# Performance work log

Hardware: AMD Instinct MI355X
Metric: run time of the kernel (lower is better)

## Reference

```python
import jax, jax.numpy as jnp
import numpy as np

NEG_SLOPE = 0.2


def gat_layer(x, adj, W, a_src, a_dst):
    # x: (C, in_dim), adj: (C, C) 0/1, W: (in_dim, H*D), a_src/a_dst: (H, D)
    C = x.shape[0]
    H, D = a_src.shape
    h = (x @ W).reshape(C, H, D)            # (C, H, D)
    hh = jnp.transpose(h, (1, 0, 2))        # (H, C, D)
    asrc = jnp.einsum('hcd,hd->hc', hh, a_src)  # (H, C)
    adst = jnp.einsum('hcd,hd->hc', hh, a_dst)  # (H, C)
    e = asrc[:, :, None] + adst[:, None, :]     # (H, C, C)
    e = jax.nn.leaky_relu(e, NEG_SLOPE)
    e = jnp.where(adj[None, :, :] == 0, -jnp.inf, e)
    attn = jax.nn.softmax(e, axis=-1)           # (H, C, C)
    out = jnp.einsum('hij,hjd->hid', attn, hh)  # (H, C, D)
    return jnp.transpose(out, (1, 0, 2)).reshape(C, H * D)


def setup_inputs() -> dict:
    key = jax.random.key(0)
    ks = jax.random.split(key, 12)
    B, doc_dim = 1024, 768
    C, label_dim = 4096, 768
    hidden, H = 512, 4
    D = hidden // H  # 128

    doc_x = jax.random.normal(ks[0], (B, doc_dim), dtype=jnp.float32)
    label_init = jax.random.normal(ks[1], (C, label_dim), dtype=jnp.float32)
    adj = jax.random.randint(ks[2], (C, C), 0, 2, dtype=jnp.int32)
    adj = adj.at[jnp.arange(C), jnp.arange(C)].set(1)  # self-loops

    def xavier(k, shape):
        fan_in, fan_out = shape[0], shape[1]
        lim = jnp.sqrt(6.0 / (fan_in + fan_out)).astype(jnp.float32)
        return jax.random.uniform(k, shape, jnp.float32, -lim, lim)

    W1 = xavier(ks[3], (label_dim, hidden))
    a_src1 = xavier(ks[4], (H, D))
    a_dst1 = xavier(ks[5], (H, D))
    W2 = xavier(ks[6], (hidden, hidden))
    a_src2 = xavier(ks[7], (H, D))
    a_dst2 = xavier(ks[8], (H, D))
    Wd = xavier(ks[9], (doc_dim, hidden))
    bd = jnp.zeros((hidden,), jnp.float32)
    return {"doc_x": doc_x, "label_init": label_init, "adj": adj,
            "W1": W1, "a_src1": a_src1, "a_dst1": a_dst1,
            "W2": W2, "a_src2": a_src2, "a_dst2": a_dst2,
            "Wd": Wd, "bd": bd}


def reference(doc_x, label_init, adj, W1, a_src1, a_dst1, W2, a_src2, a_dst2, Wd, bd):
    # doc_proj (dropout = identity in eval)
    doc_h = jax.nn.relu(doc_x @ Wd + bd)            # (B, hidden)
    # label encoder: GAT -> ELU -> GAT
    h = gat_layer(label_init, adj, W1, a_src1, a_dst1)
    h = jax.nn.elu(h)
    label_h = gat_layer(h, adj, W2, a_src2, a_dst2)  # (C, hidden)
    logits = doc_h @ label_h.T                      # (B, C)
    return logits
```

## Files before the change

kernel.cpp:

```cpp
#include <hip/hip_runtime.h>
#include <hip/hip_bf16.h>
#include <math.h>

#define BDOCS   1024
#define CNODES  4096
#define INDIM   768
#define HID     512
#define NHEAD   4
#define HDIM    128
#define NEG_SLOPE 0.2f

typedef __attribute__((ext_vector_type(8))) short short8;
typedef __attribute__((ext_vector_type(4))) float f32x4;

__device__ __forceinline__ float lrelu(float x) { return x > 0.f ? x : NEG_SLOPE * x; }

__device__ __forceinline__ short f2bf(float f) {
    union { float f; unsigned u; } v; v.f = f;
    unsigned r = (v.u + 0x7fff + ((v.u >> 16) & 1)) >> 16;
    return (short)r;
}
__device__ __forceinline__ float bf2f(short s) {
    union { float f; unsigned u; } v; v.u = ((unsigned)(unsigned short)s) << 16;
    return v.f;
}

__global__ __launch_bounds__(256)
void pack_adj(const int* __restrict__ adj, unsigned long long* __restrict__ adjb64)
{
    const int t    = threadIdx.x;
    const int gw   = blockIdx.x * 4 + (t >> 6);
    const int lane = t & 63;
    const int i  = gw >> 6;
    const int j0 = (gw & 63) * 64;
    const int a  = adj[(size_t)i * CNODES + j0 + lane];
    const unsigned long long m = __ballot(a != 0);
    if (lane == 0) adjb64[(size_t)i * 64 + (j0 >> 6)] = m;
}

__global__ __launch_bounds__(512)
void attn_prep(const float* __restrict__ hpre,
               const float* __restrict__ a_src,
               const float* __restrict__ a_dst,
               float* __restrict__ asrc, float* __restrict__ adst)
{
    const int i = blockIdx.x;
    const int t = threadIdx.x;
    __shared__ float s1[512], s2[512];
    const float hv = hpre[(size_t)i * HID + t];
    s1[t] = hv * a_src[t];
    s2[t] = hv * a_dst[t];
    __syncthreads();
    for (int s = 64; s >= 1; s >>= 1) {
        if ((t & 127) < s) { s1[t] += s1[t + s]; s2[t] += s2[t + s]; }
        __syncthreads();
    }
    if ((t & 127) == 0) {
        const int h = t >> 7;
        asrc[h * CNODES + i] = s1[t];
        adst[h * CNODES + i] = s2[t];
    }
}

__global__ __launch_bounds__(256)
void adst_max(const float* __restrict__ adst, float* __restrict__ Mh)
{
    const int h = blockIdx.x, t = threadIdx.x;
    __shared__ float red[256];
    float m = -1e30f;
    for (int j = t; j < CNODES; j += 256) m = fmaxf(m, adst[h * CNODES + j]);
    red[t] = m; __syncthreads();
    for (int s = 128; s >= 1; s >>= 1) {
        if (t < s) red[t] = fmaxf(red[t], red[t + s]);
        __syncthreads();
    }
    if (t == 0) Mh[h] = red[0];
}

__global__ __launch_bounds__(256)
void frag_T(const float* __restrict__ src, short* __restrict__ dst, int N, int K)
{
    __shared__ float tile[32][132];
    const int jc = blockIdx.x;
    const int nq = blockIdx.y;
    const int t  = threadIdx.x;
    const int KC = K >> 5;
#pragma unroll
    for (int it = 0; it < 16; it++) {
        const int e = it * 256 + t;
        const int j = e >> 7, n = e & 127;
        tile[j][n] = src[(size_t)(jc * 32 + j) * N + nq * 128 + n];
    }
    __syncthreads();
#pragma unroll
    for (int s = 0; s < 2; s++) {
        const int item = s * 256 + t;
        const int nbl = item >> 6, lane = item & 63;
        const int nr = lane & 15, kq = lane >> 4;
        short8 v;
#pragma unroll
        for (int jr = 0; jr < 8; jr++)
            v[jr] = f2bf(tile[kq * 8 + jr][nbl * 16 + nr]);
        *(short8*)&dst[((size_t)((nq * 8 + nbl) * KC + jc) * 64 + lane) * 8] = v;
    }
}

template <bool ELU>
__global__ __launch_bounds__(256)
void frag_A(const float* __restrict__ src, short* __restrict__ dst, int C)
{
    __shared__ float tile[16][132];
    const int rb = blockIdx.x, cq = blockIdx.y;
    const int t  = threadIdx.x;
    const int KC = C >> 5;
#pragma unroll
    for (int it = 0; it < 8; it++) {
        const int e = it * 256 + t;
        const int r = e >> 7, c = e & 127;
        float v = src[(size_t)(rb * 16 + r) * C + cq * 128 + c];
        if (ELU) v = v > 0.f ? v : (__expf(v) - 1.f);
        tile[r][c] = v;
    }
    __syncthreads();
    const int kcl = t >> 6, lane = t & 63;
    const int m = lane & 15, kq = lane >> 4;
    short8 v8;
#pragma unroll
    for (int j = 0; j < 8; j++) v8[j] = f2bf(tile[m][kcl * 32 + kq * 8 + j]);
    *(short8*)&dst[((size_t)(rb * KC + cq * 4 + kcl) * 64 + lane) * 8] = v8;
}

template <int KC, bool BIASRELU>
__global__ __launch_bounds__(64, 3)
void gemm_frag(const short* __restrict__ Af, const short* __restrict__ Bf,
               const float* __restrict__ bias, float* __restrict__ Cmat, int N)
{
    const int lane = threadIdx.x;
    const int mb0  = blockIdx.x * 2;
    const int nq   = blockIdx.y;

    f32x4 acc[2][8];
#pragma unroll
    for (int f = 0; f < 2; f++)
#pragma unroll
        for (int c = 0; c < 8; c++) acc[f][c] = (f32x4){0.f, 0.f, 0.f, 0.f};

    const short* ap0 = Af + (size_t)mb0 * KC * 512 + lane * 8;
    const short* ap1 = ap0 + (size_t)KC * 512;
    const short* bp  = Bf + (size_t)(nq * 8) * KC * 512 + lane * 8;

#pragma unroll 2
    for (int kc = 0; kc < KC; kc++) {
        short8 a0 = *(const short8*)(ap0 + (size_t)kc * 512);
        short8 a1 = *(const short8*)(ap1 + (size_t)kc * 512);
        short8 bf[8];
#pragma unroll
        for (int c = 0; c < 8; c++)
            bf[c] = *(const short8*)(bp + ((size_t)c * KC + kc) * 512);
#pragma unroll
        for (int c = 0; c < 8; c++) {
            acc[0][c] = __builtin_amdgcn_mfma_f32_16x16x32_bf16(a0, bf[c], acc[0][c], 0, 0, 0);
            acc[1][c] = __builtin_amdgcn_mfma_f32_16x16x32_bf16(a1, bf[c], acc[1][c], 0, 0, 0);
        }
    }

    const int col = lane & 15, q4 = lane >> 4;
#pragma unroll
    for (int f = 0; f < 2; f++)
#pragma unroll
        for (int c = 0; c < 8; c++)
#pragma unroll
            for (int r = 0; r < 4; r++) {
                const int row = (mb0 + f) * 16 + q4 * 4 + r;
                const int n   = nq * 128 + c * 16 + col;
                float v = acc[f][c][r];
                if (BIASRELU) v = fmaxf(v + bias[n], 0.f);
                Cmat[(size_t)row * N + n] = v;
            }
}

__global__ __launch_bounds__(256, 3)
void attn_pv(const short* __restrict__ hbTf,
             const unsigned int* __restrict__ adjb,
             const float* __restrict__ asrc, const float* __restrict__ adst,
             const float* __restrict__ Mh,
             float* __restrict__ part, float* __restrict__ lpart,
             int jper)
{
    const int t    = threadIdx.x;
    const int w    = t >> 6;
    const int lane = t & 63;
    const int m    = lane & 15;
    const int kq   = lane >> 4;
    const int i0   = blockIdx.x * 32;
    const int ks   = blockIdx.y;
    const int js   = ks * jper;

    const float as0 = asrc[w * CNODES + i0 + m];
    const float as1 = asrc[w * CNODES + i0 + 16 + m];
    const float mh  = Mh[w];
    const float mr0 = lrelu(as0 + mh);
    const float mr1 = lrelu(as1 + mh);
    float ls0 = 0.f, ls1 = 0.f;

    f32x4 acc[2][8];
#pragma unroll
    for (int f = 0; f < 2; f++)
#pragma unroll
        for (int c = 0; c < 8; c++) acc[f][c] = (f32x4){0.f, 0.f, 0.f, 0.f};

    const unsigned int* ar0 = adjb + (size_t)(i0 + m) * 128 + (js >> 5);
    const unsigned int* ar1 = adjb + (size_t)(i0 + 16 + m) * 128 + (js >> 5);
    const int nchunks = jper >> 5;

    for (int ch = 0; ch < nchunks; ch++) {
        const int j0 = js + ch * 32;
        const unsigned int aw0 = ar0[ch] >> (kq * 8);
        const unsigned int aw1 = ar1[ch] >> (kq * 8);
        const float4* dp = (const float4*)(adst + (size_t)w * CNODES + j0 + kq * 8);
        const float4 d0 = dp[0], d1 = dp[1];

        short8 bf[8];
        const short* bbase = hbTf + (((size_t)(w * 8) * 128 + (j0 >> 5)) * 64 + lane) * 8;
#pragma unroll
        for (int c = 0; c < 8; c++)
            bf[c] = *(const short8*)(bbase + (size_t)c * 128 * 64 * 8);

        const float dv[8] = {d0.x, d0.y, d0.z, d0.w, d1.x, d1.y, d1.z, d1.w};
        short8 a0, a1;
#pragma unroll
        for (int q = 0; q < 8; q++) {
            const unsigned b0 = (aw0 >> q) & 1u, b1 = (aw1 >> q) & 1u;
            float w0 = b0 ? __expf(lrelu(as0 + dv[q]) - mr0) : 0.f;
            float w1 = b1 ? __expf(lrelu(as1 + dv[q]) - mr1) : 0.f;
            short r0 = f2bf(w0), r1 = f2bf(w1);
            a0[q] = r0; a1[q] = r1;
            ls0 += bf2f(r0); ls1 += bf2f(r1);
        }

#pragma unroll
        for (int c = 0; c < 8; c++) {
            acc[0][c] = __builtin_amdgcn_mfma_f32_16x16x32_bf16(a0, bf[c], acc[0][c], 0, 0, 0);
            acc[1][c] = __builtin_amdgcn_mfma_f32_16x16x32_bf16(a1, bf[c], acc[1][c], 0, 0, 0);
        }
    }

    ls0 += __shfl_xor(ls0, 16); ls0 += __shfl_xor(ls0, 32);
    ls1 += __shfl_xor(ls1, 16); ls1 += __shfl_xor(ls1, 32);
    if (lane < 16) {
        lpart[((size_t)ks * NHEAD + w) * CNODES + i0 + m]      = ls0;
        lpart[((size_t)ks * NHEAD + w) * CNODES + i0 + 16 + m] = ls1;
    }

    float* pbase = part + (size_t)ks * CNODES * HID;
    const int col = lane & 15, q4 = lane >> 4;
#pragma unroll
    for (int f = 0; f < 2; f++)
#pragma unroll
        for (int c = 0; c < 8; c++)
#pragma unroll
            for (int r = 0; r < 4; r++) {
                const int row = i0 + f * 16 + q4 * 4 + r;
                pbase[(size_t)row * HID + w * HDIM + c * 16 + col] = acc[f][c][r];
            }
}

__global__ __launch_bounds__(256)
void reduce_norm(const float* __restrict__ part, const float* __restrict__ lpart,
                 float* __restrict__ outbuf, int KS)
{
    const int idx = blockIdx.x * 256 + threadIdx.x;
    const int i = idx >> 9, n = idx & 511;
    const int h = n >> 7;
    float l = 0.f, v = 0.f;
    for (int s = 0; s < KS; s++) {
        l += lpart[((size_t)s * NHEAD + h) * CNODES + i];
        v += part[(size_t)s * CNODES * HID + idx];
    }
    outbuf[idx] = v / l;
}

extern "C" void kernel_launch(void* const* d_in, const int* in_sizes, int n_in,
                              void* d_out, int out_size, void* d_ws, size_t ws_size,
                              hipStream_t stream)
{
    const float* doc_x      = (const float*)d_in[0];
    const float* label_init = (const float*)d_in[1];
    const int*   adj        = (const int*)d_in[2];
    const float* W1         = (const float*)d_in[3];
    const float* a_src1     = (const float*)d_in[4];
    const float* a_dst1     = (const float*)d_in[5];
    const float* W2         = (const float*)d_in[6];
    const float* a_src2     = (const float*)d_in[7];
    const float* a_dst2     = (const float*)d_in[8];
    const float* Wd         = (const float*)d_in[9];
    const float* bd         = (const float*)d_in[10];
    float*       out        = (float*)d_out;

    char* wsb = (char*)d_ws;
    size_t off = 0;
    auto alloc = [&](size_t bytes) -> char* {
        char* p = wsb + off;
        off = (off + bytes + 255) & ~(size_t)255;
        return p;
    };

    float* doc_h = (float*)alloc((size_t)BDOCS * HID * 4);
    float* buf1  = (float*)alloc((size_t)CNODES * HID * 4);
    float* buf2  = (float*)alloc((size_t)CNODES * HID * 4);
    float* asrc  = (float*)alloc(NHEAD * CNODES * 4);
    float* adst  = (float*)alloc(NHEAD * CNODES * 4);
    float* Mh    = (float*)alloc(256);
    float* lpart = (float*)alloc((size_t)4 * NHEAD * CNODES * 4);
    unsigned int* adjb = (unsigned int*)alloc((size_t)CNODES * 128 * 4);
    short* hbTf  = (short*)alloc((size_t)CNODES * HID * 2);
    short* Wdf   = (short*)alloc((size_t)INDIM * HID * 2);
    short* W1f   = (short*)alloc((size_t)INDIM * HID * 2);
    short* W2f   = (short*)alloc((size_t)HID * HID * 2);
    short* dxf   = (short*)alloc((size_t)BDOCS * INDIM * 2);
    char*  reg   = alloc((size_t)9 << 20);
    short* Af_li = (short*)reg;
    short* Af2   = (short*)reg;
    short* lhf   = (short*)(reg + ((size_t)4 << 20));
    short* dhf   = (short*)(reg + ((size_t)8 << 20));
    float* part  = (float*)(wsb + off);

    int KS = 4;
    const size_t slice_bytes = (size_t)CNODES * HID * 4;
    while (KS > 1 && off + (size_t)KS * slice_bytes > ws_size) KS >>= 1;
    const int jper = CNODES / KS;

    const dim3 blk(256);

    pack_adj<<<CNODES * CNODES / 64 / 4, blk, 0, stream>>>(adj, (unsigned long long*)adjb);
    frag_T<<<dim3(INDIM / 32, HID / 128), blk, 0, stream>>>(Wd, Wdf, HID, INDIM);
    frag_T<<<dim3(INDIM / 32, HID / 128), blk, 0, stream>>>(W1, W1f, HID, INDIM);
    frag_T<<<dim3(HID / 32, HID / 128), blk, 0, stream>>>(W2, W2f, HID, HID);
    frag_A<false><<<dim3(BDOCS / 16, INDIM / 128), blk, 0, stream>>>(doc_x, dxf, INDIM);
    frag_A<false><<<dim3(CNODES / 16, INDIM / 128), blk, 0, stream>>>(label_init, Af_li, INDIM);

    gemm_frag<INDIM / 32, false><<<dim3(CNODES / 32, HID / 128), 64, 0, stream>>>(Af_li, W1f, nullptr, buf1, HID);

    gemm_frag<INDIM / 32, true><<<dim3(BDOCS / 32, HID / 128), 64, 0, stream>>>(dxf, Wdf, bd, doc_h, HID);
    frag_A<false><<<dim3(BDOCS / 16, HID / 128), blk, 0, stream>>>(doc_h, dhf, HID);

    attn_prep<<<CNODES, 512, 0, stream>>>(buf1, a_src1, a_dst1, asrc, adst);
    adst_max<<<NHEAD, 256, 0, stream>>>(adst, Mh);
    frag_T<<<dim3(CNODES / 32, HID / 128), blk, 0, stream>>>(buf1, hbTf, HID, CNODES);
    attn_pv<<<dim3(CNODES / 32, KS), blk, 0, stream>>>(hbTf, adjb, asrc, adst, Mh, part, lpart, jper);
    reduce_norm<<<CNODES * HID / 256, blk, 0, stream>>>(part, lpart, buf2, KS);

    frag_A<true><<<dim3(CNODES / 16, HID / 128), blk, 0, stream>>>(buf2, Af2, HID);
    gemm_frag<HID / 32, false><<<dim3(CNODES / 32, HID / 128), 64, 0, stream>>>(Af2, W2f, nullptr, buf1, HID);

    attn_prep<<<CNODES, 512, 0, stream>>>(buf1, a_src2, a_dst2, asrc, adst);
    adst_max<<<NHEAD, 256, 0, stream>>>(adst, Mh);
    frag_T<<<dim3(CNODES / 32, HID / 128), blk, 0, stream>>>(buf1, hbTf, HID, CNODES);
    attn_pv<<<dim3(CNODES / 32, KS), blk, 0, stream>>>(hbTf, adjb, asrc, adst, Mh, part, lpart, jper);
    reduce_norm<<<CNODES * HID / 256, blk, 0, stream>>>(part, lpart, buf2, KS);

    frag_A<false><<<dim3(CNODES / 16, HID / 128), blk, 0, stream>>>(buf2, lhf, HID);
    gemm_frag<HID / 32, false><<<dim3(BDOCS / 32, CNODES / 128), 64, 0, stream>>>(dhf, lhf, nullptr, out, CNODES);
}
```

Measured before the change: 371.0 us.

## Fuse GEMM epilogues with attention prep, factor exp out of attention loop

```diff
diff --git a/kernel.cpp b/kernel.cpp
--- a/kernel.cpp
+++ b/kernel.cpp
@@ -20,9 +20,15 @@
     unsigned r = (v.u + 0x7fff + ((v.u >> 16) & 1)) >> 16;
     return (short)r;
 }
-__device__ __forceinline__ float bf2f(short s) {
-    union { float f; unsigned u; } v; v.u = ((unsigned)(unsigned short)s) << 16;
-    return v.f;
+__device__ __forceinline__ unsigned pk2(float a, float b) {
+    union { float f; unsigned u; } x, y; x.f = a; y.f = b;
+    unsigned lo = (x.u + 0x7fff + ((x.u >> 16) & 1)) >> 16;
+    unsigned hi = (y.u + 0x7fff + ((y.u >> 16) & 1)) >> 16;
+    return lo | (hi << 16);
+}
+__device__ __forceinline__ short hup(float f) {
+    union { float f; unsigned u; } v; v.f = f;
+    return (short)((v.u + 0x8000) >> 16);
 }
 
 __global__ __launch_bounds__(256)
@@ -38,28 +44,236 @@
     if (lane == 0) adjb64[(size_t)i * 64 + (j0 >> 6)] = m;
 }
 
-__global__ __launch_bounds__(512)
-void attn_prep(const float* __restrict__ hpre,
-               const float* __restrict__ a_src,
-               const float* __restrict__ a_dst,
-               float* __restrict__ asrc, float* __restrict__ adst)
-{
-    const int i = blockIdx.x;
-    const int t = threadIdx.x;
-    __shared__ float s1[512], s2[512];
-    const float hv = hpre[(size_t)i * HID + t];
-    s1[t] = hv * a_src[t];
-    s2[t] = hv * a_dst[t];
+__global__ __launch_bounds__(256)
+void frag_T(const float* __restrict__ src, short* __restrict__ dst, int N, int K)
+{
+    __shared__ float tile[32][132];
+    const int jc = blockIdx.x;
+    const int nq = blockIdx.y;
+    const int t  = threadIdx.x;
+    const int KC = K >> 5;
+#pragma unroll
+    for (int it = 0; it < 16; it++) {
+        const int e = it * 256 + t;
+        const int j = e >> 7, n = e & 127;
+        tile[j][n] = src[(size_t)(jc * 32 + j) * N + nq * 128 + n];
+    }
     __syncthreads();
-    for (int s = 64; s >= 1; s >>= 1) {
-        if ((t & 127) < s) { s1[t] += s1[t + s]; s2[t] += s2[t + s]; }
-        __syncthreads();
-    }
-    if ((t & 127) == 0) {
-        const int h = t >> 7;
-        asrc[h * CNODES + i] = s1[t];
-        adst[h * CNODES + i] = s2[t];
-    }
+#pragma unroll
+    for (int s = 0; s < 2; s++) {
+        const int item = s * 256 + t;
+        const int nbl = item >> 6, lane = item & 63;
+        const int nr = lane & 15, kq = lane >> 4;
+        short8 v;
+#pragma unroll
+        for (int jr = 0; jr < 8; jr++)
+            v[jr] = f2bf(tile[kq * 8 + jr][nbl * 16 + nr]);
+        *(short8*)&dst[((size_t)((nq * 8 + nbl) * KC + jc) * 64 + lane) * 8] = v;
+    }
+}
+
+__global__ __launch_bounds__(256)
+void frag_A(const float* __restrict__ src, short* __restrict__ dst, int C)
+{
+    __shared__ float tile[16][132];
+    const int rb = blockIdx.x, cq = blockIdx.y;
+    const int t  = threadIdx.x;
+    const int KC = C >> 5;
+#pragma unroll
+    for (int it = 0; it < 8; it++) {
+        const int e = it * 256 + t;
+        const int r = e >> 7, c = e & 127;
+        tile[r][c] = src[(size_t)(rb * 16 + r) * C + cq * 128 + c];
+    }
+    __syncthreads();
+    const int kcl = t >> 6, lane = t & 63;
+    const int m = lane & 15, kq = lane >> 4;
+    short8 v8;
+#pragma unroll
+    for (int j = 0; j < 8; j++) v8[j] = f2bf(tile[m][kcl * 32 + kq * 8 + j]);
+    *(short8*)&dst[((size_t)(rb * KC + cq * 4 + kcl) * 64 + lane) * 8] = v8;
+}
+
+template <int KC>
+__global__ __launch_bounds__(64)
+void gemm_hpre(const short* __restrict__ Af, const short* __restrict__ Bf,
+               const float* __restrict__ a_src, const float* __restrict__ a_dst,
+               short* __restrict__ hbTf, float* __restrict__ asrc, float* __restrict__ adst)
+{
+    __shared__ __align__(16) short tileT[128][56];
+    const int lane = threadIdx.x;
+    const int mb0  = blockIdx.x * 2;
+    const int nq   = blockIdx.y;
+    const int i0   = blockIdx.x * 32;
+
+    f32x4 acc[2][8];
+#pragma unroll
+    for (int f = 0; f < 2; f++)
+#pragma unroll
+        for (int c = 0; c < 8; c++) acc[f][c] = (f32x4){0.f, 0.f, 0.f, 0.f};
+
+    const short* ap0 = Af + (size_t)mb0 * KC * 512 + lane * 8;
+    const short* ap1 = ap0 + (size_t)KC * 512;
+    const short* bp  = Bf + (size_t)(nq * 8) * KC * 512 + lane * 8;
+
+#pragma unroll 2
+    for (int kc = 0; kc < KC; kc++) {
+        short8 a0 = *(const short8*)(ap0 + (size_t)kc * 512);
+        short8 a1 = *(const short8*)(ap1 + (size_t)kc * 512);
+        short8 bf[8];
+#pragma unroll
+        for (int c = 0; c < 8; c++)
+            bf[c] = *(const short8*)(bp + ((size_t)c * KC + kc) * 512);
+#pragma unroll
+        for (int c = 0; c < 8; c++) {
+            acc[0][c] = __builtin_amdgcn_mfma_f32_16x16x32_bf16(a0, bf[c], acc[0][c], 0, 0, 0);
+            acc[1][c] = __builtin_amdgcn_mfma_f32_16x16x32_bf16(a1, bf[c], acc[1][c], 0, 0, 0);
+        }
+    }
+
+    const int col = lane & 15, q4 = lane >> 4;
+
+#pragma unroll
+    for (int f = 0; f < 2; f++)
+#pragma unroll
+        for (int c = 0; c < 8; c++) {
+            unsigned d0 = pk2(acc[f][c][0], acc[f][c][1]);
+            unsigned d1 = pk2(acc[f][c][2], acc[f][c][3]);
+            uint2 u; u.x = d0; u.y = d1;
+            *(uint2*)&tileT[c * 16 + col][f * 16 + q4 * 4] = u;
+        }
+    __syncthreads();
+    {
+        const int nr = lane & 15, kq = lane >> 4;
+#pragma unroll
+        for (int nbl = 0; nbl < 8; nbl++) {
+            short8 v = *(const short8*)&tileT[nbl * 16 + nr][kq * 8];
+            *(short8*)&hbTf[(((size_t)(nq * 8 + nbl) * (CNODES / 32) + blockIdx.x) * 64 + lane) * 8] = v;
+        }
+    }
+
+    float ssrc[2][4] = {}, sdst[2][4] = {};
+#pragma unroll
+    for (int c = 0; c < 8; c++) {
+        const float vs = a_src[nq * 128 + c * 16 + col];
+        const float vd = a_dst[nq * 128 + c * 16 + col];
+#pragma unroll
+        for (int f = 0; f < 2; f++)
+#pragma unroll
+            for (int r = 0; r < 4; r++) {
+                ssrc[f][r] += acc[f][c][r] * vs;
+                sdst[f][r] += acc[f][c][r] * vd;
+            }
+    }
+#pragma unroll
+    for (int mask = 1; mask <= 8; mask <<= 1)
+#pragma unroll
+        for (int f = 0; f < 2; f++)
+#pragma unroll
+            for (int r = 0; r < 4; r++) {
+                ssrc[f][r] += __shfl_xor(ssrc[f][r], mask);
+                sdst[f][r] += __shfl_xor(sdst[f][r], mask);
+            }
+    if (col == 0) {
+#pragma unroll
+        for (int f = 0; f < 2; f++)
+#pragma unroll
+            for (int r = 0; r < 4; r++) {
+                const int row = i0 + f * 16 + q4 * 4 + r;
+                asrc[nq * CNODES + row] = ssrc[f][r];
+                adst[nq * CNODES + row] = sdst[f][r];
+            }
+    }
+}
+
+template <int KC>
+__global__ __launch_bounds__(64)
+void gemm_doc(const short* __restrict__ Af, const short* __restrict__ Bf,
+              const float* __restrict__ bias, short* __restrict__ dhf)
+{
+    __shared__ __align__(16) short tile[16][128];
+    const int lane = threadIdx.x;
+    const int mb = blockIdx.x;
+    const int nq = blockIdx.y;
+
+    f32x4 acc[8];
+#pragma unroll
+    for (int c = 0; c < 8; c++) acc[c] = (f32x4){0.f, 0.f, 0.f, 0.f};
+
+    const short* ap = Af + (size_t)mb * KC * 512 + lane * 8;
+    const short* bp = Bf + (size_t)(nq * 8) * KC * 512 + lane * 8;
+
+#pragma unroll 2
+    for (int kc = 0; kc < KC; kc++) {
+        short8 a = *(const short8*)(ap + (size_t)kc * 512);
+#pragma unroll
+        for (int c = 0; c < 8; c++) {
+            short8 bf = *(const short8*)(bp + ((size_t)c * KC + kc) * 512);
+            acc[c] = __builtin_amdgcn_mfma_f32_16x16x32_bf16(a, bf, acc[c], 0, 0, 0);
+        }
+    }
+
+    const int col = lane & 15, q4 = lane >> 4;
+#pragma unroll
+    for (int c = 0; c < 8; c++)
+#pragma unroll
+        for (int r = 0; r < 4; r++) {
+            float v = fmaxf(acc[c][r] + bias[nq * 128 + c * 16 + col], 0.f);
+            tile[q4 * 4 + r][c * 16 + col] = f2bf(v);
+        }
+    __syncthreads();
+    const int m = lane & 15, kq = lane >> 4;
+#pragma unroll
+    for (int kcl = 0; kcl < 4; kcl++) {
+        short8 v = *(const short8*)&tile[m][kcl * 32 + kq * 8];
+        *(short8*)&dhf[(((size_t)mb * 16 + nq * 4 + kcl) * 64 + lane) * 8] = v;
+    }
+}
+
+template <int KC>
+__global__ __launch_bounds__(64)
+void gemm_frag(const short* __restrict__ Af, const short* __restrict__ Bf,
+               float* __restrict__ Cmat, int N)
+{
+    const int lane = threadIdx.x;
+    const int mb0  = blockIdx.x * 2;
+    const int nq   = blockIdx.y;
+
+    f32x4 acc[2][8];
+#pragma unroll
+    for (int f = 0; f < 2; f++)
+#pragma unroll
+        for (int c = 0; c < 8; c++) acc[f][c] = (f32x4){0.f, 0.f, 0.f, 0.f};
+
+    const short* ap0 = Af + (size_t)mb0 * KC * 512 + lane * 8;
+    const short* ap1 = ap0 + (size_t)KC * 512;
+    const short* bp  = Bf + (size_t)(nq * 8) * KC * 512 + lane * 8;
+
+#pragma unroll 2
+    for (int kc = 0; kc < KC; kc++) {
+        short8 a0 = *(const short8*)(ap0 + (size_t)kc * 512);
+        short8 a1 = *(const short8*)(ap1 + (size_t)kc * 512);
+        short8 bf[8];
+#pragma unroll
+        for (int c = 0; c < 8; c++)
+            bf[c] = *(const short8*)(bp + ((size_t)c * KC + kc) * 512);
+#pragma unroll
+        for (int c = 0; c < 8; c++) {
+            acc[0][c] = __builtin_amdgcn_mfma_f32_16x16x32_bf16(a0, bf[c], acc[0][c], 0, 0, 0);
+            acc[1][c] = __builtin_amdgcn_mfma_f32_16x16x32_bf16(a1, bf[c], acc[1][c], 0, 0, 0);
+        }
+    }
+
+    const int col = lane & 15, q4 = lane >> 4;
+#pragma unroll
+    for (int f = 0; f < 2; f++)
+#pragma unroll
+        for (int c = 0; c < 8; c++)
+#pragma unroll
+            for (int r = 0; r < 4; r++) {
+                const int row = (mb0 + f) * 16 + q4 * 4 + r;
+                Cmat[(size_t)row * N + nq * 128 + c * 16 + col] = acc[f][c][r];
+            }
 }
 
 __global__ __launch_bounds__(256)
@@ -78,111 +292,21 @@
 }
 
 __global__ __launch_bounds__(256)
-void frag_T(const float* __restrict__ src, short* __restrict__ dst, int N, int K)
-{
-    __shared__ float tile[32][132];
-    const int jc = blockIdx.x;
-    const int nq = blockIdx.y;
-    const int t  = threadIdx.x;
-    const int KC = K >> 5;
-#pragma unroll
-    for (int it = 0; it < 16; it++) {
-        const int e = it * 256 + t;
-        const int j = e >> 7, n = e & 127;
-        tile[j][n] = src[(size_t)(jc * 32 + j) * N + nq * 128 + n];
-    }
-    __syncthreads();
-#pragma unroll
-    for (int s = 0; s < 2; s++) {
-        const int item = s * 256 + t;
-        const int nbl = item >> 6, lane = item & 63;
-        const int nr = lane & 15, kq = lane >> 4;
-        short8 v;
-#pragma unroll
-        for (int jr = 0; jr < 8; jr++)
-            v[jr] = f2bf(tile[kq * 8 + jr][nbl * 16 + nr]);
-        *(short8*)&dst[((size_t)((nq * 8 + nbl) * KC + jc) * 64 + lane) * 8] = v;
-    }
-}
-
-template <bool ELU>
-__global__ __launch_bounds__(256)
-void frag_A(const float* __restrict__ src, short* __restrict__ dst, int C)
-{
-    __shared__ float tile[16][132];
-    const int rb = blockIdx.x, cq = blockIdx.y;
-    const int t  = threadIdx.x;
-    const int KC = C >> 5;
-#pragma unroll
-    for (int it = 0; it < 8; it++) {
-        const int e = it * 256 + t;
-        const int r = e >> 7, c = e & 127;
-        float v = src[(size_t)(rb * 16 + r) * C + cq * 128 + c];
-        if (ELU) v = v > 0.f ? v : (__expf(v) - 1.f);
-        tile[r][c] = v;
-    }
-    __syncthreads();
-    const int kcl = t >> 6, lane = t & 63;
-    const int m = lane & 15, kq = lane >> 4;
-    short8 v8;
-#pragma unroll
-    for (int j = 0; j < 8; j++) v8[j] = f2bf(tile[m][kcl * 32 + kq * 8 + j]);
-    *(short8*)&dst[((size_t)(rb * KC + cq * 4 + kcl) * 64 + lane) * 8] = v8;
-}
-
-template <int KC, bool BIASRELU>
-__global__ __launch_bounds__(64, 3)
-void gemm_frag(const short* __restrict__ Af, const short* __restrict__ Bf,
-               const float* __restrict__ bias, float* __restrict__ Cmat, int N)
-{
-    const int lane = threadIdx.x;
-    const int mb0  = blockIdx.x * 2;
-    const int nq   = blockIdx.y;
-
-    f32x4 acc[2][8];
-#pragma unroll
-    for (int f = 0; f < 2; f++)
-#pragma unroll
-        for (int c = 0; c < 8; c++) acc[f][c] = (f32x4){0.f, 0.f, 0.f, 0.f};
-
-    const short* ap0 = Af + (size_t)mb0 * KC * 512 + lane * 8;
-    const short* ap1 = ap0 + (size_t)KC * 512;
-    const short* bp  = Bf + (size_t)(nq * 8) * KC * 512 + lane * 8;
-
-#pragma unroll 2
-    for (int kc = 0; kc < KC; kc++) {
-        short8 a0 = *(const short8*)(ap0 + (size_t)kc * 512);
-        short8 a1 = *(const short8*)(ap1 + (size_t)kc * 512);
-        short8 bf[8];
-#pragma unroll
-        for (int c = 0; c < 8; c++)
-            bf[c] = *(const short8*)(bp + ((size_t)c * KC + kc) * 512);
-#pragma unroll
-        for (int c = 0; c < 8; c++) {
-            acc[0][c] = __builtin_amdgcn_mfma_f32_16x16x32_bf16(a0, bf[c], acc[0][c], 0, 0, 0);
-            acc[1][c] = __builtin_amdgcn_mfma_f32_16x16x32_bf16(a1, bf[c], acc[1][c], 0, 0, 0);
-        }
-    }
-
-    const int col = lane & 15, q4 = lane >> 4;
-#pragma unroll
-    for (int f = 0; f < 2; f++)
-#pragma unroll
-        for (int c = 0; c < 8; c++)
-#pragma unroll
-            for (int r = 0; r < 4; r++) {
-                const int row = (mb0 + f) * 16 + q4 * 4 + r;
-                const int n   = nq * 128 + c * 16 + col;
-                float v = acc[f][c][r];
-                if (BIASRELU) v = fmaxf(v + bias[n], 0.f);
-                Cmat[(size_t)row * N + n] = v;
-            }
-}
-
-__global__ __launch_bounds__(256, 3)
+void exp_dst(const float* __restrict__ adst, const float* __restrict__ Mh,
+             float* __restrict__ E1, float* __restrict__ E2)
+{
+    const int idx = blockIdx.x * 256 + threadIdx.x;
+    const int h = idx >> 12;
+    const float d = adst[idx] - Mh[h];
+    E1[idx] = __expf(d);
+    E2[idx] = __expf(0.2f * d);
+}
+
+__global__ __launch_bounds__(256, 2)
 void attn_pv(const short* __restrict__ hbTf,
              const unsigned int* __restrict__ adjb,
-             const float* __restrict__ asrc, const float* __restrict__ adst,
+             const float* __restrict__ asrc,
+             const float* __restrict__ E1, const float* __restrict__ E2,
              const float* __restrict__ Mh,
              float* __restrict__ part, float* __restrict__ lpart,
              int jper)
@@ -196,18 +320,24 @@
     const int ks   = blockIdx.y;
     const int js   = ks * jper;
 
+    const float mh  = Mh[w];
     const float as0 = asrc[w * CNODES + i0 + m];
     const float as1 = asrc[w * CNODES + i0 + 16 + m];
-    const float mh  = Mh[w];
-    const float mr0 = lrelu(as0 + mh);
-    const float mr1 = lrelu(as1 + mh);
-    float ls0 = 0.f, ls1 = 0.f;
-
-    f32x4 acc[2][8];
-#pragma unroll
-    for (int f = 0; f < 2; f++)
+    const float mr0 = lrelu(as0 + mh), mr1 = lrelu(as1 + mh);
+    const float A10 = __expf(as0 + mh - mr0),        A11 = __expf(as1 + mh - mr1);
+    const float A20 = __expf(0.2f * (as0 + mh) - mr0), A21 = __expf(0.2f * (as1 + mh) - mr1);
+    const float T00 = __expf(-as0 - mh),             T01 = __expf(-as1 - mh);
+
+    f32x4 acc[2][8], accO[2];
+#pragma unroll
+    for (int f = 0; f < 2; f++) {
+        accO[f] = (f32x4){0.f, 0.f, 0.f, 0.f};
 #pragma unroll
         for (int c = 0; c < 8; c++) acc[f][c] = (f32x4){0.f, 0.f, 0.f, 0.f};
+    }
+    short8 ones;
+#pragma unroll
+    for (int q = 0; q < 8; q++) ones[q] = (short)0x3F80;
 
     const unsigned int* ar0 = adjb + (size_t)(i0 + m) * 128 + (js >> 5);
     const unsigned int* ar1 = adjb + (size_t)(i0 + 16 + m) * 128 + (js >> 5);
@@ -217,8 +347,12 @@
         const int j0 = js + ch * 32;
         const unsigned int aw0 = ar0[ch] >> (kq * 8);
         const unsigned int aw1 = ar1[ch] >> (kq * 8);
-        const float4* dp = (const float4*)(adst + (size_t)w * CNODES + j0 + kq * 8);
-        const float4 d0 = dp[0], d1 = dp[1];
+        const float4* p1 = (const float4*)(E1 + (size_t)w * CNODES + j0 + kq * 8);
+        const float4* p2 = (const float4*)(E2 + (size_t)w * CNODES + j0 + kq * 8);
+        const float4 x0 = p1[0], x1 = p1[1];
+        const float4 y0 = p2[0], y1 = p2[1];
+        const float e1v[8] = {x0.x, x0.y, x0.z, x0.w, x1.x, x1.y, x1.z, x1.w};
+        const float e2v[8] = {y0.x, y0.y, y0.z, y0.w, y1.x, y1.y, y1.z, y1.w};
 
         short8 bf[8];
         const short* bbase = hbTf + (((size_t)(w * 8) * 128 + (j0 >> 5)) * 64 + lane) * 8;
@@ -226,16 +360,17 @@
         for (int c = 0; c < 8; c++)
             bf[c] = *(const short8*)(bbase + (size_t)c * 128 * 64 * 8);
 
-        const float dv[8] = {d0.x, d0.y, d0.z, d0.w, d1.x, d1.y, d1.z, d1.w};
         short8 a0, a1;
 #pragma unroll
         for (int q = 0; q < 8; q++) {
-            const unsigned b0 = (aw0 >> q) & 1u, b1 = (aw1 >> q) & 1u;
-            float w0 = b0 ? __expf(lrelu(as0 + dv[q]) - mr0) : 0.f;
-            float w1 = b1 ? __expf(lrelu(as1 + dv[q]) - mr1) : 0.f;
-            short r0 = f2bf(w0), r1 = f2bf(w1);
-            a0[q] = r0; a1[q] = r1;
-            ls0 += bf2f(r0); ls1 += bf2f(r1);
+            const float e1 = e1v[q], e2 = e2v[q];
+            const bool c0 = e1 > T00, c1 = e1 > T01;
+            float w0 = (c0 ? A10 : A20) * (c0 ? e1 : e2);
+            float w1 = (c1 ? A11 : A21) * (c1 ? e1 : e2);
+            w0 = ((aw0 >> q) & 1u) ? w0 : 0.f;
+            w1 = ((aw1 >> q) & 1u) ? w1 : 0.f;
+            a0[q] = hup(w0);
+            a1[q] = hup(w1);
         }
 
 #pragma unroll
@@ -243,17 +378,20 @@
             acc[0][c] = __builtin_amdgcn_mfma_f32_16x16x32_bf16(a0, bf[c], acc[0][c], 0, 0, 0);
             acc[1][c] = __builtin_amdgcn_mfma_f32_16x16x32_bf16(a1, bf[c], acc[1][c], 0, 0, 0);
         }
-    }
-
-    ls0 += __shfl_xor(ls0, 16); ls0 += __shfl_xor(ls0, 32);
-    ls1 += __shfl_xor(ls1, 16); ls1 += __shfl_xor(ls1, 32);
-    if (lane < 16) {
-        lpart[((size_t)ks * NHEAD + w) * CNODES + i0 + m]      = ls0;
-        lpart[((size_t)ks * NHEAD + w) * CNODES + i0 + 16 + m] = ls1;
+        accO[0] = __builtin_amdgcn_mfma_f32_16x16x32_bf16(a0, ones, accO[0], 0, 0, 0);
+        accO[1] = __builtin_amdgcn_mfma_f32_16x16x32_bf16(a1, ones, accO[1], 0, 0, 0);
+    }
+
+    const int col = lane & 15, q4 = lane >> 4;
+    if (col == 0) {
+#pragma unroll
+        for (int f = 0; f < 2; f++)
+#pragma unroll
+            for (int r = 0; r < 4; r++)
+                lpart[((size_t)ks * NHEAD + w) * CNODES + i0 + f * 16 + q4 * 4 + r] = accO[f][r];
     }
 
     float* pbase = part + (size_t)ks * CNODES * HID;
-    const int col = lane & 15, q4 = lane >> 4;
 #pragma unroll
     for (int f = 0; f < 2; f++)
 #pragma unroll
@@ -265,19 +403,38 @@
             }
 }
 
+template <bool ELU>
 __global__ __launch_bounds__(256)
-void reduce_norm(const float* __restrict__ part, const float* __restrict__ lpart,
-                 float* __restrict__ outbuf, int KS)
-{
-    const int idx = blockIdx.x * 256 + threadIdx.x;
-    const int i = idx >> 9, n = idx & 511;
-    const int h = n >> 7;
-    float l = 0.f, v = 0.f;
+void reduce_norm_frag(const float* __restrict__ part, const float* __restrict__ lpart,
+                      short* __restrict__ dst, int KS)
+{
+    const int t = threadIdx.x;
+    const int W = blockIdx.x * 4 + (t >> 6);
+    const int lane = t & 63;
+    const int rb = W >> 4, kc = W & 15;
+    const int m = lane & 15, kq = lane >> 4;
+    const int i = rb * 16 + m;
+    const int n0 = kc * 32 + kq * 8;
+    const int h = kc >> 2;
+
+    float v[8] = {};
+    float l = 0.f;
     for (int s = 0; s < KS; s++) {
+        const float* p = part + (size_t)s * CNODES * HID + (size_t)i * HID + n0;
+        const float4 a = ((const float4*)p)[0], b = ((const float4*)p)[1];
+        v[0] += a.x; v[1] += a.y; v[2] += a.z; v[3] += a.w;
+        v[4] += b.x; v[5] += b.y; v[6] += b.z; v[7] += b.w;
         l += lpart[((size_t)s * NHEAD + h) * CNODES + i];
-        v += part[(size_t)s * CNODES * HID + idx];
-    }
-    outbuf[idx] = v / l;
+    }
+    const float inv = 1.0f / l;
+    short8 o;
+#pragma unroll
+    for (int q = 0; q < 8; q++) {
+        float x = v[q] * inv;
+        if (ELU) x = x > 0.f ? x : (__expf(x) - 1.f);
+        o[q] = f2bf(x);
+    }
+    *(short8*)&dst[((size_t)(rb * 16 + kc) * 64 + lane) * 8] = o;
 }
 
 extern "C" void kernel_launch(void* const* d_in, const int* in_sizes, int n_in,
@@ -305,24 +462,22 @@
         return p;
     };
 
-    float* doc_h = (float*)alloc((size_t)BDOCS * HID * 4);
-    float* buf1  = (float*)alloc((size_t)CNODES * HID * 4);
-    float* buf2  = (float*)alloc((size_t)CNODES * HID * 4);
     float* asrc  = (float*)alloc(NHEAD * CNODES * 4);
     float* adst  = (float*)alloc(NHEAD * CNODES * 4);
     float* Mh    = (float*)alloc(256);
-    float* lpart = (float*)alloc((size_t)4 * NHEAD * CNODES * 4);
+    float* E1    = (float*)alloc(NHEAD * CNODES * 4);
+    float* E2    = (float*)alloc(NHEAD * CNODES * 4);
+    float* lpart = (float*)alloc((size_t)8 * NHEAD * CNODES * 4);
     unsigned int* adjb = (unsigned int*)alloc((size_t)CNODES * 128 * 4);
     short* hbTf  = (short*)alloc((size_t)CNODES * HID * 2);
     short* Wdf   = (short*)alloc((size_t)INDIM * HID * 2);
     short* W1f   = (short*)alloc((size_t)INDIM * HID * 2);
     short* W2f   = (short*)alloc((size_t)HID * HID * 2);
     short* dxf   = (short*)alloc((size_t)BDOCS * INDIM * 2);
-    char*  reg   = alloc((size_t)9 << 20);
-    short* Af_li = (short*)reg;
-    short* Af2   = (short*)reg;
-    short* lhf   = (short*)(reg + ((size_t)4 << 20));
-    short* dhf   = (short*)(reg + ((size_t)8 << 20));
+    short* Af_li = (short*)alloc((size_t)CNODES * INDIM * 2);
+    short* Af2   = (short*)alloc((size_t)CNODES * HID * 2);
+    short* lhf   = (short*)alloc((size_t)CNODES * HID * 2);
+    short* dhf   = (short*)alloc((size_t)BDOCS * HID * 2);
     float* part  = (float*)(wsb + off);
 
     int KS = 4;
@@ -336,29 +491,26 @@
     frag_T<<<dim3(INDIM / 32, HID / 128), blk, 0, stream>>>(Wd, Wdf, HID, INDIM);
     frag_T<<<dim3(INDIM / 32, HID / 128), blk, 0, stream>>>(W1, W1f, HID, INDIM);
     frag_T<<<dim3(HID / 32, HID / 128), blk, 0, stream>>>(W2, W2f, HID, HID);
-    frag_A<false><<<dim3(BDOCS / 16, INDIM / 128), blk, 0, stream>>>(doc_x, dxf, INDIM);
-    frag_A<false><<<dim3(CNODES / 16, INDIM / 128), blk, 0, stream>>>(label_init, Af_li, INDIM);
-
-    gemm_frag<INDIM / 32, false><<<dim3(CNODES / 32, HID / 128), 64, 0, stream>>>(Af_li, W1f, nullptr, buf1, HID);
-
-    gemm_frag<INDIM / 32, true><<<dim3(BDOCS / 32, HID / 128), 64, 0, stream>>>(dxf, Wdf, bd, doc_h, HID);
-    frag_A<false><<<dim3(BDOCS / 16, HID / 128), blk, 0, stream>>>(doc_h, dhf, HID);
-
-    attn_prep<<<CNODES, 512, 0, stream>>>(buf1, a_src1, a_dst1, asrc, adst);
+    frag_A<<<dim3(BDOCS / 16, INDIM / 128), blk, 0, stream>>>(doc_x, dxf, INDIM);
+    frag_A<<<dim3(CNODES / 16, INDIM / 128), blk, 0, stream>>>(label_init, Af_li, INDIM);
+
+    gemm_doc<INDIM / 32><<<dim3(BDOCS / 16, HID / 128), 64, 0, stream>>>(dxf, Wdf, bd, dhf);
+
+    gemm_hpre<INDIM / 32><<<dim3(CNODES / 32, NHEAD), 64, 0, stream>>>(
+        Af_li, W1f, a_src1, a_dst1, hbTf, asrc, adst);
+
     adst_max<<<NHEAD, 256, 0, stream>>>(adst, Mh);
-    frag_T<<<dim3(CNODES / 32, HID / 128), blk, 0, stream>>>(buf1, hbTf, HID, CNODES);
-    attn_pv<<<dim3(CNODES / 32, KS), blk, 0, stream>>>(hbTf, adjb, asrc, adst, Mh, part, lpart, jper);
-    reduce_norm<<<CNODES * HID / 256, blk, 0, stream>>>(part, lpart, buf2, KS);
-
-    frag_A<true><<<dim3(CNODES / 16, HID / 128), blk, 0, stream>>>(buf2, Af2, HID);
-    gemm_frag<HID / 32, false><<<dim3(CNODES / 32, HID / 128), 64, 0, stream>>>(Af2, W2f, nullptr, buf1, HID);
-
-    attn_prep<<<CNODES, 512, 0, stream>>>(buf1, a_src2, a_dst2, asrc, adst);
+    exp_dst<<<NHEAD * CNODES / 256, blk, 0, stream>>>(adst, Mh, E1, E2);
+    attn_pv<<<dim3(CNODES / 32, KS), blk, 0, stream>>>(hbTf, adjb, asrc, E1, E2, Mh, part, lpart, jper);
+    reduce_norm_frag<true><<<CNODES * HID / 256 / 8, blk, 0, stream>>>(part, lpart, Af2, KS);
+
+    gemm_hpre<HID / 32><<<dim3(CNODES / 32, NHEAD), 64, 0, stream>>>(
+        Af2, W2f, a_src2, a_dst2, hbTf, asrc, adst);
+
     adst_max<<<NHEAD, 256, 0, stream>>>(adst, Mh);
-    frag_T<<<dim3(CNODES / 32, HID / 128), blk, 0, stream>>>(buf1, hbTf, HID, CNODES);
-    attn_pv<<<dim3(CNODES / 32, KS), blk, 0, stream>>>(hbTf, adjb, asrc, adst, Mh, part, lpart, jper);
-    reduce_norm<<<CNODES * HID / 256, blk, 0, stream>>>(part, lpart, buf2, KS);
-
-    frag_A<false><<<dim3(CNODES / 16, HID / 128), blk, 0, stream>>>(buf2, lhf, HID);
-    gemm_frag<HID / 32, false><<<dim3(BDOCS / 32, CNODES / 128), 64, 0, stream>>>(dhf, lhf, nullptr, out, CNODES);
-}
+    exp_dst<<<NHEAD * CNODES / 256, blk, 0, stream>>>(adst, Mh, E1, E2);
+    attn_pv<<<dim3(CNODES / 32, KS), blk, 0, stream>>>(hbTf, adjb, asrc, E1, E2, Mh, part, lpart, jper);
+    reduce_norm_frag<false><<<CNODES * HID / 256 / 8, blk, 0, stream>>>(part, lpart, lhf, KS);
+
+    gemm_frag<HID / 32><<<dim3(BDOCS / 32, CNODES / 128), 64, 0, stream>>>(dhf, lhf, out, CNODES);
+}
```

Result: slower. 411.6 us (+10.9%).
